# Kernel optimization log

Hardware: AMD Instinct MI355X
Metric: run time of the kernel (lower is better)

Reference implementation:

```python
import jax, jax.numpy as jnp
import numpy as np

L = 256  # hardcoded heatmap size in the original module
EPS = 1e-6
SIGMA = 1.0 / 3.0
BOX_T = 0.5
MASK_T = 0.1


def _gen_mask(Yp):
    """Faithful vectorized version of get_box_pos + make_heatmap for one [L,L] map."""
    M = jnp.where(Yp > BOX_T, Yp, 0.0)
    rows = jnp.sum(M, axis=1) > 0  # scan over rows (dim 0)
    cols = jnp.sum(M, axis=0) > 0  # scan over cols (dim 1)
    left = jnp.argmax(rows)                 # first nonzero row
    right = jnp.argmax(rows[::-1])          # offset of last nonzero row from the end
    up = jnp.argmax(cols)                   # first nonzero col
    down = jnp.argmax(cols[::-1])           # offset of last nonzero col from the end
    x_r = (right - left) // 2
    y_r = (down - up) // 2
    gt0 = (left + x_r).astype(jnp.float32)  # compared against coord0 = column index y
    gt1 = (up + y_r).astype(jnp.float32)    # compared against coord1 = row index x
    # make_heatmap: heatmap[x, y, :] = [y, x]
    ys = jnp.arange(L, dtype=jnp.float32)[None, :]  # coord0 over columns
    xs = jnp.arange(L, dtype=jnp.float32)[:, None]  # coord1 over rows
    d0 = (ys - gt0) / x_r.astype(jnp.float32)
    d1 = (xs - gt1) / y_r.astype(jnp.float32)
    h = d0 ** 4 + d1 ** 4                  # ((v^2)^2 summed over last dim)
    h = jnp.exp(-h / (2.0 * SIGMA) ** 2)
    return (h > MASK_T).astype(Yp.dtype)


def _per_sample(Yp, Yg):
    gen = _gen_mask(Yp)
    use_gt = jnp.max(Yg) > 0
    Yg_eff = jnp.where(use_gt, Yg, gen)
    positive = jnp.sum(Yg_eff * Yp)
    negative = jnp.sum((1.0 - Yg_eff) * Yp)
    return negative / (positive + EPS)


def setup_inputs() -> dict:
    key = jax.random.key(0)
    k1, k2, k3 = jax.random.split(key, 3)
    B = 512
    # predictions: background in [0, 0.4), a bright blob > 0.5 so box-finding works
    Y_pred = jax.random.uniform(k1, (B, L, L), dtype=jnp.float32) * 0.4
    blob = 0.6 + 0.4 * jax.random.uniform(k3, (B, 40, 80), dtype=jnp.float32)
    Y_pred = Y_pred.at[:, 100:140, 80:160].set(blob)
    # binary gt masks; zero out first half of batch to trigger the generated-mask branch
    Y_gt = (jax.random.uniform(k2, (B, L, L)) > 0.95).astype(jnp.float32)
    Y_gt = Y_gt.at[: B // 2].set(0.0)
    return {"Y_pred": Y_pred, "Y_gt": Y_gt}


def reference(Y_pred, Y_gt):
    ratios = jax.vmap(_per_sample)(Y_pred, Y_gt)  # [B]
    total = jnp.sum(ratios)
    N = Y_gt.shape[0]
    return jnp.where(total == 0, 0.0, jnp.log(total) / N)
```

## Files before the change

### kernel.cpp

```cpp
#include <hip/hip_runtime.h>
#include <math.h>

constexpr int L = 256;
constexpr float EPS = 1e-6f;

__device__ inline float wave_sum(float v) {
#pragma unroll
    for (int off = 32; off > 0; off >>= 1) v += __shfl_down(v, off, 64);
    return v;
}

__global__ __launch_bounds__(256) void per_sample_kernel(
    const float* __restrict__ Yp, const float* __restrict__ Yg,
    float* __restrict__ ratios) {
    const int b = blockIdx.x;
    const int t = threadIdx.x;
    const float* yp = Yp + (size_t)b * L * L;
    const float* yg = Yg + (size_t)b * L * L;
    const float4* yp4 = (const float4*)yp;
    const float4* yg4 = (const float4*)yg;

    __shared__ unsigned rowmask[8], colmask[8];
    __shared__ float part1[4], part2[4];
    __shared__ int s_anyg;
    __shared__ float s_sum_p, s_sum_pg;
    __shared__ int s_box[4];
    __shared__ float s_par[4];
    __shared__ int s_empty;

    if (t < 8) { rowmask[t] = 0u; colmask[t] = 0u; }
    if (t == 0) s_anyg = 0;
    __syncthreads();

    float sum_p = 0.f, sum_pg = 0.f;
    int anyg = 0;
#pragma unroll 4
    for (int k = 0; k < 64; ++k) {
        const int j = t + (k << 8);
        const float4 p = yp4[j];
        const float4 g = yg4[j];
        sum_p  += (p.x + p.y) + (p.z + p.w);
        sum_pg += p.x * g.x + p.y * g.y + p.z * g.z + p.w * g.w;
        anyg |= (g.x > 0.f) | (g.y > 0.f) | (g.z > 0.f) | (g.w > 0.f);
        const bool bx = p.x > 0.5f, by = p.y > 0.5f,
                   bz = p.z > 0.5f, bw = p.w > 0.5f;
        if (bx | by | bz | bw) {
            const int row = j >> 6;
            atomicOr(&rowmask[row >> 5], 1u << (row & 31));
            const int c0 = (j << 2) & 255;
            const unsigned bits =
                ((unsigned)bx | ((unsigned)by << 1) | ((unsigned)bz << 2) |
                 ((unsigned)bw << 3)) << (c0 & 31);
            atomicOr(&colmask[c0 >> 5], bits);
        }
    }
    if (anyg) atomicOr(&s_anyg, 1);

    float w1 = wave_sum(sum_p);
    float w2 = wave_sum(sum_pg);
    const int wave = t >> 6, lane = t & 63;
    if (lane == 0) { part1[wave] = w1; part2[wave] = w2; }
    __syncthreads();

    if (t == 0) {
        s_sum_p  = part1[0] + part1[1] + part1[2] + part1[3];
        s_sum_pg = part2[0] + part2[1] + part2[2] + part2[3];
        int first_r = 0, last_r = 0, first_c = 0, last_c = 0;
        bool any_r = false, any_c = false;
        for (int i = 0; i < 8; ++i) {
            unsigned w = rowmask[i];
            if (w) {
                if (!any_r) { first_r = i * 32 + __builtin_ffs((int)w) - 1; any_r = true; }
                last_r = i * 32 + 31 - __builtin_clz(w);
            }
            unsigned wc = colmask[i];
            if (wc) {
                if (!any_c) { first_c = i * 32 + __builtin_ffs((int)wc) - 1; any_c = true; }
                last_c = i * 32 + 31 - __builtin_clz(wc);
            }
        }
        const int left  = any_r ? first_r : 0;
        const int right = any_r ? (L - 1 - last_r) : 0;
        const int up    = any_c ? first_c : 0;
        const int down  = any_c ? (L - 1 - last_c) : 0;
        const int x_r = (right - left) >> 1;
        const int y_r = (down - up) >> 1;
        const float gt0 = (float)(left + x_r);
        const float gt1 = (float)(up + y_r);
        if (s_anyg || x_r == 0 || y_r == 0) {
            s_empty = 1;
        } else {
            s_empty = 0;
            s_par[0] = gt0; s_par[1] = gt1;
            s_par[2] = 1.f / (float)x_r; s_par[3] = 1.f / (float)y_r;
            const float mx = fabsf((float)x_r) * 1.02f + 1.f;
            const float my = fabsf((float)y_r) * 1.02f + 1.f;
            s_box[0] = max(0, (int)floorf(gt0 - mx));
            s_box[1] = min(L - 1, (int)ceilf(gt0 + mx));
            s_box[2] = max(0, (int)floorf(gt1 - my));
            s_box[3] = min(L - 1, (int)ceilf(gt1 + my));
        }
    }
    __syncthreads();

    float pos_gen = 0.f;
    if (!s_empty) {
        const int cl = s_box[0], ch = s_box[1], rl = s_box[2], rh = s_box[3];
        const int W = ch - cl + 1, H = rh - rl + 1;
        const float gt0 = s_par[0], gt1 = s_par[1];
        const float inv_xr = s_par[2], inv_yr = s_par[3];
        for (int idx = t; idx < W * H; idx += 256) {
            const int r = rl + idx / W;
            const int c = cl + idx % W;
            float d0 = ((float)c - gt0) * inv_xr;
            float d1 = ((float)r - gt1) * inv_yr;
            d0 *= d0; d0 *= d0;
            d1 *= d1; d1 *= d1;
            const float h = __expf(-2.25f * (d0 + d1));
            if (h > 0.1f) pos_gen += yp[r * L + c];
        }
    }
    float w3 = wave_sum(pos_gen);
    if (lane == 0) part1[wave] = w3;
    __syncthreads();
    if (t == 0) {
        const float positive =
            s_anyg ? s_sum_pg : (part1[0] + part1[1] + part1[2] + part1[3]);
        ratios[b] = (s_sum_p - positive) / (positive + EPS);
    }
}

__global__ __launch_bounds__(256) void finalize_kernel(
    const float* __restrict__ ratios, float* __restrict__ out, int B) {
    float v = 0.f;
    for (int i = threadIdx.x; i < B; i += 256) v += ratios[i];
    v = wave_sum(v);
    __shared__ float part[4];
    const int wave = threadIdx.x >> 6, lane = threadIdx.x & 63;
    if (lane == 0) part[wave] = v;
    __syncthreads();
    if (threadIdx.x == 0) {
        const float total = part[0] + part[1] + part[2] + part[3];
        out[0] = (total == 0.f) ? 0.f : logf(total) / (float)B;
    }
}

extern "C" void kernel_launch(void* const* d_in, const int* in_sizes, int n_in,
                              void* d_out, int out_size, void* d_ws, size_t ws_size,
                              hipStream_t stream) {
    const float* Yp = (const float*)d_in[0];
    const float* Yg = (const float*)d_in[1];
    const int B = in_sizes[0] / (L * L);
    float* ratios = (float*)d_ws;
    per_sample_kernel<<<B, 256, 0, stream>>>(Yp, Yg, ratios);
    finalize_kernel<<<1, 256, 0, stream>>>(ratios, (float*)d_out, B);
}
```

Baseline: 276.0 us.

## Split per-sample reduction across four blocks with global atomic records and second pass

Each sample's streaming reduction is split across four blocks. The blocks combine their partial sums, any-gt flag and row/column masks into a per-sample global record using atomics. A second 64-thread kernel reads the record, computes the box, and sums the generated-mask region. The aim is to raise block count and memory-level parallelism for the bandwidth-bound pass. The cost is two extra launches (zeroing and pass2), global atomics, and a nondeterministic float summation order.

```diff
diff --git a/kernel.cpp b/kernel.cpp
--- a/kernel.cpp
+++ b/kernel.cpp
@@ -3,6 +3,9 @@
 
 constexpr int L = 256;
 constexpr float EPS = 1e-6f;
+constexpr int SPLIT = 4;
+constexpr int REC_WORDS = 20;
+
 
 __device__ inline float wave_sum(float v) {
 #pragma unroll
@@ -10,32 +13,31 @@
     return v;
 }
 
-__global__ __launch_bounds__(256) void per_sample_kernel(
+__global__ __launch_bounds__(256) void zero_kernel(unsigned* __restrict__ w, int n) {
+    const int i = blockIdx.x * 256 + threadIdx.x;
+    if (i < n) w[i] = 0u;
+}
+
+__global__ __launch_bounds__(256) void pass1_kernel(
     const float* __restrict__ Yp, const float* __restrict__ Yg,
-    float* __restrict__ ratios) {
-    const int b = blockIdx.x;
+    unsigned* __restrict__ recs) {
+    const int blk = blockIdx.x;
+    const int b = blk >> 2;
+    const int s = blk & 3;
     const int t = threadIdx.x;
-    const float* yp = Yp + (size_t)b * L * L;
-    const float* yg = Yg + (size_t)b * L * L;
-    const float4* yp4 = (const float4*)yp;
-    const float4* yg4 = (const float4*)yg;
+    const float4* yp4 = (const float4*)(Yp + (size_t)b * L * L) + s * 4096;
+    const float4* yg4 = (const float4*)(Yg + (size_t)b * L * L) + s * 4096;
+    unsigned* rec = recs + b * REC_WORDS;
 
     __shared__ unsigned rowmask[8], colmask[8];
     __shared__ float part1[4], part2[4];
-    __shared__ int s_anyg;
-    __shared__ float s_sum_p, s_sum_pg;
-    __shared__ int s_box[4];
-    __shared__ float s_par[4];
-    __shared__ int s_empty;
-
     if (t < 8) { rowmask[t] = 0u; colmask[t] = 0u; }
-    if (t == 0) s_anyg = 0;
     __syncthreads();
 
     float sum_p = 0.f, sum_pg = 0.f;
     int anyg = 0;
 #pragma unroll 4
-    for (int k = 0; k < 64; ++k) {
+    for (int k = 0; k < 16; ++k) {
         const int j = t + (k << 8);
         const float4 p = yp4[j];
         const float4 g = yg4[j];
@@ -45,71 +47,90 @@
         const bool bx = p.x > 0.5f, by = p.y > 0.5f,
                    bz = p.z > 0.5f, bw = p.w > 0.5f;
         if (bx | by | bz | bw) {
-            const int row = j >> 6;
+            const int gj = s * 4096 + j;
+            const int row = gj >> 6;
             atomicOr(&rowmask[row >> 5], 1u << (row & 31));
-            const int c0 = (j << 2) & 255;
+            const int c0 = (gj << 2) & 255;
             const unsigned bits =
                 ((unsigned)bx | ((unsigned)by << 1) | ((unsigned)bz << 2) |
                  ((unsigned)bw << 3)) << (c0 & 31);
             atomicOr(&colmask[c0 >> 5], bits);
         }
     }
-    if (anyg) atomicOr(&s_anyg, 1);
+    const int wave = t >> 6, lane = t & 63;
+    const int wany = __any(anyg);
+    if (lane == 0 && wany) atomicOr(&rec[2], 1u);
 
     float w1 = wave_sum(sum_p);
     float w2 = wave_sum(sum_pg);
-    const int wave = t >> 6, lane = t & 63;
     if (lane == 0) { part1[wave] = w1; part2[wave] = w2; }
     __syncthreads();
 
     if (t == 0) {
-        s_sum_p  = part1[0] + part1[1] + part1[2] + part1[3];
-        s_sum_pg = part2[0] + part2[1] + part2[2] + part2[3];
-        int first_r = 0, last_r = 0, first_c = 0, last_c = 0;
-        bool any_r = false, any_c = false;
-        for (int i = 0; i < 8; ++i) {
-            unsigned w = rowmask[i];
-            if (w) {
-                if (!any_r) { first_r = i * 32 + __builtin_ffs((int)w) - 1; any_r = true; }
-                last_r = i * 32 + 31 - __builtin_clz(w);
-            }
-            unsigned wc = colmask[i];
-            if (wc) {
-                if (!any_c) { first_c = i * 32 + __builtin_ffs((int)wc) - 1; any_c = true; }
-                last_c = i * 32 + 31 - __builtin_clz(wc);
-            }
+        atomicAdd((float*)&rec[0], part1[0] + part1[1] + part1[2] + part1[3]);
+        atomicAdd((float*)&rec[1], part2[0] + part2[1] + part2[2] + part2[3]);
+    } else if (t >= 32 && t < 40) {
+        const unsigned m = rowmask[t - 32];
+        if (m) atomicOr(&rec[3 + (t - 32)], m);
+    } else if (t >= 40 && t < 48) {
+        const unsigned m = colmask[t - 40];
+        if (m) atomicOr(&rec[11 + (t - 40)], m);
+    }
+}
+
+__global__ __launch_bounds__(64) void pass2_kernel(
+    const float* __restrict__ Yp, const unsigned* __restrict__ recs,
+    float* __restrict__ ratios) {
+    const int b = blockIdx.x;
+    const int lane = threadIdx.x;
+    const unsigned* rec = recs + b * REC_WORDS;
+    const float* yp = Yp + (size_t)b * L * L;
+
+    const float sum_p  = ((const float*)rec)[0];
+    const float sum_pg = ((const float*)rec)[1];
+    const unsigned anyg = rec[2];
+
+    int first_r = 0, last_r = 0, first_c = 0, last_c = 0;
+    bool any_r = false, any_c = false;
+#pragma unroll
+    for (int i = 0; i < 8; ++i) {
+        const unsigned wr = rec[3 + i];
+        if (wr) {
+            if (!any_r) { first_r = i * 32 + __builtin_ffs((int)wr) - 1; any_r = true; }
+            last_r = i * 32 + 31 - __builtin_clz(wr);
         }
-        const int left  = any_r ? first_r : 0;
-        const int right = any_r ? (L - 1 - last_r) : 0;
-        const int up    = any_c ? first_c : 0;
-        const int down  = any_c ? (L - 1 - last_c) : 0;
-        const int x_r = (right - left) >> 1;
-        const int y_r = (down - up) >> 1;
-        const float gt0 = (float)(left + x_r);
-        const float gt1 = (float)(up + y_r);
-        if (s_anyg || x_r == 0 || y_r == 0) {
-            s_empty = 1;
-        } else {
-            s_empty = 0;
-            s_par[0] = gt0; s_par[1] = gt1;
-            s_par[2] = 1.f / (float)x_r; s_par[3] = 1.f / (float)y_r;
-            const float mx = fabsf((float)x_r) * 1.02f + 1.f;
-            const float my = fabsf((float)y_r) * 1.02f + 1.f;
-            s_box[0] = max(0, (int)floorf(gt0 - mx));
-            s_box[1] = min(L - 1, (int)ceilf(gt0 + mx));
-            s_box[2] = max(0, (int)floorf(gt1 - my));
-            s_box[3] = min(L - 1, (int)ceilf(gt1 + my));
+        const unsigned wc = rec[11 + i];
+        if (wc) {
+            if (!any_c) { first_c = i * 32 + __builtin_ffs((int)wc) - 1; any_c = true; }
+            last_c = i * 32 + 31 - __builtin_clz(wc);
         }
     }
-    __syncthreads();
+    const int left  = any_r ? first_r : 0;
+    const int right = any_r ? (L - 1 - last_r) : 0;
+    const int up    = any_c ? first_c : 0;
+    const int down  = any_c ? (L - 1 - last_c) : 0;
+    const int x_r = (right - left) >> 1;
+    const int y_r = (down - up) >> 1;
+    const float gt0 = (float)(left + x_r);
+    const float gt1 = (float)(up + y_r);
 
-    float pos_gen = 0.f;
-    if (!s_empty) {
-        const int cl = s_box[0], ch = s_box[1], rl = s_box[2], rh = s_box[3];
+    float positive;
+    if (anyg) {
+        positive = sum_pg;
+    } else if (x_r == 0 || y_r == 0) {
+        positive = 0.f;
+    } else {
+        const float inv_xr = 1.f / (float)x_r;
+        const float inv_yr = 1.f / (float)y_r;
+        const float mx = fabsf((float)x_r) * 1.02f + 1.f;
+        const float my = fabsf((float)y_r) * 1.02f + 1.f;
+        const int cl = max(0, (int)floorf(gt0 - mx));
+        const int ch = min(L - 1, (int)ceilf(gt0 + mx));
+        const int rl = max(0, (int)floorf(gt1 - my));
+        const int rh = min(L - 1, (int)ceilf(gt1 + my));
         const int W = ch - cl + 1, H = rh - rl + 1;
-        const float gt0 = s_par[0], gt1 = s_par[1];
-        const float inv_xr = s_par[2], inv_yr = s_par[3];
-        for (int idx = t; idx < W * H; idx += 256) {
+        float pos = 0.f;
+        for (int idx = lane; idx < W * H; idx += 64) {
             const int r = rl + idx / W;
             const int c = cl + idx % W;
             float d0 = ((float)c - gt0) * inv_xr;
@@ -117,17 +138,11 @@
             d0 *= d0; d0 *= d0;
             d1 *= d1; d1 *= d1;
             const float h = __expf(-2.25f * (d0 + d1));
-            if (h > 0.1f) pos_gen += yp[r * L + c];
+            if (h > 0.1f) pos += yp[r * L + c];
         }
+        positive = wave_sum(pos);
     }
-    float w3 = wave_sum(pos_gen);
-    if (lane == 0) part1[wave] = w3;
-    __syncthreads();
-    if (t == 0) {
-        const float positive =
-            s_anyg ? s_sum_pg : (part1[0] + part1[1] + part1[2] + part1[3]);
-        ratios[b] = (s_sum_p - positive) / (positive + EPS);
-    }
+    if (lane == 0) ratios[b] = (sum_p - positive) / (positive + EPS);
 }
 
 __global__ __launch_bounds__(256) void finalize_kernel(
@@ -151,7 +166,11 @@
     const float* Yp = (const float*)d_in[0];
     const float* Yg = (const float*)d_in[1];
     const int B = in_sizes[0] / (L * L);
-    float* ratios = (float*)d_ws;
-    per_sample_kernel<<<B, 256, 0, stream>>>(Yp, Yg, ratios);
+    unsigned* recs = (unsigned*)d_ws;
+    float* ratios = (float*)((char*)d_ws + (size_t)B * REC_WORDS * 4);
+    const int nz = B * REC_WORDS;
+    zero_kernel<<<(nz + 255) / 256, 256, 0, stream>>>(recs, nz);
+    pass1_kernel<<<B * SPLIT, 256, 0, stream>>>(Yp, Yg, recs);
+    pass2_kernel<<<B, 64, 0, stream>>>(Yp, recs, ratios);
     finalize_kernel<<<1, 256, 0, stream>>>(ratios, (float*)d_out, B);
 }
```

New measurement: 285.2 us. +3.4%, slower.
